# Kernel tuning notes

Measured on AMD Instinct MI355X. Metric: run time of the kernel, lower is better.

## Reference

```python
import jax, jax.numpy as jnp
import numpy as np
from jax import lax

N, E, F, H, B = 16384, 262144, 32, 128, 16
DI, DS, DC, DTR = 256, 16, 4, 8   # Mamba: d_inner=expand*H, d_state, d_conv, dt_rank=ceil(H/16)
NS, NC = 512, 8                   # num_stations, num line colors
EPS = 1e-5


def _forward(node_features, edge_index, batch, W_in, b_in, W_g1, b_g1, W_g2, b_g2,
             W_inproj, conv_w, conv_b, W_xproj, W_dt, b_dt, A_log, D_p, W_out,
             gamma, beta, Wc, bc, Wh, bh, Wt, bt, Wp1, bp1, Wp2, bp2, Wd, bd, Ws, bs):
    def gcn(x, W, b):
        # GCNConv with self-loops and symmetric normalization
        loops = jnp.arange(N)
        s = jnp.concatenate([edge_index[0], loops])
        d = jnp.concatenate([edge_index[1], loops])
        deg = jax.ops.segment_sum(jnp.ones(s.shape[0], x.dtype), d, num_segments=N)
        dinv = jnp.where(deg > 0, lax.rsqrt(deg), 0.0)
        xw = x @ W
        msg = xw[s] * (dinv[s] * dinv[d])[:, None]
        return jax.ops.segment_sum(msg, d, num_segments=N) + b

    h = jax.nn.relu(node_features @ W_in + b_in)
    h = jax.nn.relu(gcn(h, W_g1, b_g1))
    h_gnn = jax.nn.relu(gcn(h, W_g2, b_g2))

    # --- Mamba block over the node sequence (batch dim of 1, seq_len = N) ---
    xz = h_gnn @ W_inproj                      # (N, 2*DI)
    x, z = xz[:, :DI], xz[:, DI:]
    xp = jnp.pad(x, ((DC - 1, 0), (0, 0)))     # causal depthwise conv1d
    xc = conv_b + sum(xp[k:k + N] * conv_w[:, k] for k in range(DC))
    x = jax.nn.silu(xc)
    dbl = x @ W_xproj                          # (N, DTR + 2*DS)
    dt = jax.nn.softplus(dbl[:, :DTR] @ W_dt + b_dt)   # (N, DI)
    Bm = dbl[:, DTR:DTR + DS]                  # (N, DS)
    Cm = dbl[:, DTR + DS:]                     # (N, DS)
    A = -jnp.exp(A_log)                        # (DI, DS)
    dA = jnp.exp(dt[:, :, None] * A[None])     # (N, DI, DS)
    dBx = dt[:, :, None] * Bm[:, None, :] * x[:, :, None]

    def step(hst, t):
        dA_t, dBx_t, C_t = t
        hst = dA_t * hst + dBx_t               # (DI, DS)
        return hst, hst @ C_t                  # (DI,)

    _, ys = lax.scan(step, jnp.zeros((DI, DS), x.dtype), (dA, dBx, Cm))
    y = (ys + D_p * x) * jax.nn.silu(z)
    h_mamba = y @ W_out                        # (N, H)

    # residual + LayerNorm
    hh = h_gnn + h_mamba
    mu = hh.mean(-1, keepdims=True)
    var = ((hh - mu) ** 2).mean(-1, keepdims=True)
    h_final = (hh - mu) * lax.rsqrt(var + EPS) * gamma + beta

    # global_mean_pool per graph
    counts = jax.ops.segment_sum(jnp.ones(N, h_final.dtype), batch, num_segments=B)
    ge = jax.ops.segment_sum(h_final, batch, num_segments=B) / jnp.maximum(counts, 1.0)[:, None]

    # critic + all policy heads, concatenated: [1,4,3,NS,NS,NS,NC]
    return jnp.concatenate([ge @ Wc + bc, ge @ Wh + bh, ge @ Wt + bt,
                            ge @ Wp1 + bp1, ge @ Wp2 + bp2, ge @ Wd + bd,
                            ge @ Ws + bs], axis=-1)


def setup_inputs() -> dict:
    key = jax.random.key(0)
    ks = list(jax.random.split(key, 20))
    p = lambda i, shape, s=0.02: jax.random.normal(ks[i], shape, jnp.float32) * s
    return dict(
        node_features=jax.random.normal(ks[0], (N, F), jnp.float32),
        edge_index=jax.random.randint(ks[1], (2, E), 0, N),
        batch=jnp.sort(jax.random.randint(ks[2], (N,), 0, B)),
        W_in=p(3, (F, H)), b_in=jnp.zeros((H,), jnp.float32),
        W_g1=p(4, (H, H)), b_g1=jnp.zeros((H,), jnp.float32),
        W_g2=p(5, (H, H)), b_g2=jnp.zeros((H,), jnp.float32),
        W_inproj=p(6, (H, 2 * DI)),
        conv_w=p(7, (DI, DC)), conv_b=jnp.zeros((DI,), jnp.float32),
        W_xproj=p(8, (DI, DTR + 2 * DS)),
        W_dt=p(9, (DTR, DI)), b_dt=jnp.full((DI,), -4.0, jnp.float32),
        A_log=jnp.log(jnp.broadcast_to(jnp.arange(1.0, DS + 1.0, dtype=jnp.float32), (DI, DS))),
        D_p=jnp.ones((DI,), jnp.float32),
        W_out=p(10, (DI, H)),
        gamma=jnp.ones((H,), jnp.float32), beta=jnp.zeros((H,), jnp.float32),
        Wc=p(11, (H, 1)), bc=jnp.zeros((1,), jnp.float32),
        Wh=p(12, (H, 4)), bh=jnp.zeros((4,), jnp.float32),
        Wt=p(13, (H, 3)), bt=jnp.zeros((3,), jnp.float32),
        Wp1=p(14, (H, NS)), bp1=jnp.zeros((NS,), jnp.float32),
        Wp2=p(15, (H, NS)), bp2=jnp.zeros((NS,), jnp.float32),
        Wd=p(16, (H, NS)), bd=jnp.zeros((NS,), jnp.float32),
        Ws=p(17, (H, NC)), bs=jnp.zeros((NC,), jnp.float32),
    )


def reference(node_features, edge_index, batch, W_in, b_in, W_g1, b_g1, W_g2, b_g2,
              W_inproj, conv_w, conv_b, W_xproj, W_dt, b_dt, A_log, D_p, W_out,
              gamma, beta, Wc, bc, Wh, bh, Wt, bt, Wp1, bp1, Wp2, bp2, Wd, bd, Ws, bs):
    return _forward(node_features, edge_index, batch, W_in, b_in, W_g1, b_g1, W_g2, b_g2,
                    W_inproj, conv_w, conv_b, W_xproj, W_dt, b_dt, A_log, D_p, W_out,
                    gamma, beta, Wc, bc, Wh, bh, Wt, bt, Wp1, bp1, Wp2, bp2, Wd, bd, Ws, bs)
```

## Files before the change

kernel.cpp:

```cpp
#include <hip/hip_runtime.h>
#include <math.h>

#define NN 16384
#define EE 262144
#define FF 32
#define HH 128
#define BB 16
#define DI 256
#define DS 16
#define DC 4
#define DTR 8
#define OUTW 1552
#define NCH 256
#define CHLEN 64
#define NG 8
#define GL 32

__device__ __forceinline__ float siluf(float v) { return v / (1.f + __expf(-v)); }
__device__ __forceinline__ float softplusf(float v) {
    return fmaxf(v, 0.f) + log1pf(expf(-fabsf(v)));
}

__global__ void deg_kernel(const int* __restrict__ dst, int* __restrict__ cnt) {
    int e = blockIdx.x * blockDim.x + threadIdx.x;
    if (e < EE) atomicAdd(&cnt[dst[e]], 1);
}

__global__ __launch_bounds__(1024) void prefix_kernel(const int* __restrict__ cnt,
                                                      int* __restrict__ rowptr,
                                                      int* __restrict__ cursor,
                                                      float* __restrict__ dinv) {
    __shared__ int part[1024];
    int tid = threadIdx.x;
    int4 c4[4];
#pragma unroll
    for (int j = 0; j < 4; j++) c4[j] = ((const int4*)cnt)[tid * 4 + j];
    int v[16] = {c4[0].x, c4[0].y, c4[0].z, c4[0].w, c4[1].x, c4[1].y, c4[1].z, c4[1].w,
                 c4[2].x, c4[2].y, c4[2].z, c4[2].w, c4[3].x, c4[3].y, c4[3].z, c4[3].w};
    int s = 0;
#pragma unroll
    for (int j = 0; j < 16; j++) s += v[j];
    part[tid] = s;
    __syncthreads();
    for (int off = 1; off < 1024; off <<= 1) {
        int t = (tid >= off) ? part[tid - off] : 0;
        __syncthreads();
        part[tid] += t;
        __syncthreads();
    }
    int running = part[tid] - s;
    int rp[16];
    float dv[16];
#pragma unroll
    for (int j = 0; j < 16; j++) {
        rp[j] = running;
        running += v[j];
        dv[j] = rsqrtf((float)(v[j] + 1));
    }
#pragma unroll
    for (int j = 0; j < 4; j++) {
        int4 r4; r4.x = rp[j*4]; r4.y = rp[j*4+1]; r4.z = rp[j*4+2]; r4.w = rp[j*4+3];
        ((int4*)rowptr)[tid * 4 + j] = r4;
        ((int4*)cursor)[tid * 4 + j] = r4;
        float4 d4; d4.x = dv[j*4]; d4.y = dv[j*4+1]; d4.z = dv[j*4+2]; d4.w = dv[j*4+3];
        ((float4*)dinv)[tid * 4 + j] = d4;
    }
    if (tid == 1023) rowptr[NN] = part[1023];
}

__global__ void scatter_kernel(const int* __restrict__ src, const int* __restrict__ dst,
                               int* __restrict__ cursor, int* __restrict__ col) {
    int e = blockIdx.x * blockDim.x + threadIdx.x;
    if (e < EE) {
        int d = dst[e];
        int pos = atomicAdd(&cursor[d], 1);
        col[pos] = src[e];
    }
}

__global__ __launch_bounds__(256) void gemm_k(const float* __restrict__ A,
                                              const float* __restrict__ B,
                                              const float* __restrict__ bias,
                                              float* __restrict__ C,
                                              int M, int Nn, int K, int act) {
    __shared__ float As[16][68];
    __shared__ float Bs[16][68];
    int tid = threadIdx.x;
    int m0 = blockIdx.y * 64;
    int n0 = blockIdx.x * 64;
    int ty = tid >> 4, tx = tid & 15;
    float acc[4][4] = {{0.f}};
    for (int k0 = 0; k0 < K; k0 += 16) {
#pragma unroll
        for (int l = 0; l < 4; l++) {
            int idx = tid + l * 256;
            int i = idx >> 4, j = idx & 15;
            As[j][i] = A[(size_t)(m0 + i) * K + k0 + j];
        }
#pragma unroll
        for (int l = 0; l < 4; l++) {
            int idx = tid + l * 256;
            int i = idx >> 6, j = idx & 63;
            int n = n0 + j;
            Bs[i][j] = (n < Nn) ? B[(size_t)(k0 + i) * Nn + n] : 0.f;
        }
        __syncthreads();
#pragma unroll
        for (int kk = 0; kk < 16; kk++) {
            float4 a4 = *(const float4*)&As[kk][ty * 4];
            float4 b4 = *(const float4*)&Bs[kk][tx * 4];
            float av[4] = {a4.x, a4.y, a4.z, a4.w};
            float bv[4] = {b4.x, b4.y, b4.z, b4.w};
#pragma unroll
            for (int r = 0; r < 4; r++)
#pragma unroll
                for (int c = 0; c < 4; c++) acc[r][c] = fmaf(av[r], bv[c], acc[r][c]);
        }
        __syncthreads();
    }
    int nb = n0 + tx * 4;
    if (nb < Nn) {
        float4 bi4 = {0.f, 0.f, 0.f, 0.f};
        if (bias) bi4 = *(const float4*)&bias[nb];
#pragma unroll
        for (int r = 0; r < 4; r++) {
            int m = m0 + ty * 4 + r;
            float4 v;
            v.x = acc[r][0] + bi4.x; v.y = acc[r][1] + bi4.y;
            v.z = acc[r][2] + bi4.z; v.w = acc[r][3] + bi4.w;
            if (act == 1) {
                v.x = fmaxf(v.x, 0.f); v.y = fmaxf(v.y, 0.f);
                v.z = fmaxf(v.z, 0.f); v.w = fmaxf(v.w, 0.f);
            }
            *(float4*)&C[(size_t)m * Nn + nb] = v;
        }
    }
}

__global__ __launch_bounds__(256) void gemm_at(const float* __restrict__ AT,
                                               const float* __restrict__ B,
                                               float* __restrict__ C,
                                               int M, int Nn, int K) {
    __shared__ float As[16][68];
    __shared__ float Bs[16][68];
    int tid = threadIdx.x;
    int m0 = blockIdx.y * 64;
    int n0 = blockIdx.x * 64;
    int ty = tid >> 4, tx = tid & 15;
    float acc[4][4] = {{0.f}};
    for (int k0 = 0; k0 < K; k0 += 16) {
#pragma unroll
        for (int l = 0; l < 4; l++) {
            int idx = tid + l * 256;
            int kk = idx >> 6, i = idx & 63;
            As[kk][i] = AT[(size_t)(k0 + kk) * M + m0 + i];
        }
#pragma unroll
        for (int l = 0; l < 4; l++) {
            int idx = tid + l * 256;
            int i = idx >> 6, j = idx & 63;
            int n = n0 + j;
            Bs[i][j] = (n < Nn) ? B[(size_t)(k0 + i) * Nn + n] : 0.f;
        }
        __syncthreads();
#pragma unroll
        for (int kk = 0; kk < 16; kk++) {
            float4 a4 = *(const float4*)&As[kk][ty * 4];
            float4 b4 = *(const float4*)&Bs[kk][tx * 4];
            float av[4] = {a4.x, a4.y, a4.z, a4.w};
            float bv[4] = {b4.x, b4.y, b4.z, b4.w};
#pragma unroll
            for (int r = 0; r < 4; r++)
#pragma unroll
                for (int c = 0; c < 4; c++) acc[r][c] = fmaf(av[r], bv[c], acc[r][c]);
        }
        __syncthreads();
    }
    int nb = n0 + tx * 4;
    if (nb < Nn) {
#pragma unroll
        for (int r = 0; r < 4; r++) {
            int m = m0 + ty * 4 + r;
            float4 v;
            v.x = acc[r][0]; v.y = acc[r][1]; v.z = acc[r][2]; v.w = acc[r][3];
            *(float4*)&C[(size_t)m * Nn + nb] = v;
        }
    }
}

__global__ void gcn_gather(const float* __restrict__ xw, const int* __restrict__ rowptr,
                           const int* __restrict__ col, const float* __restrict__ dinv,
                           const float* __restrict__ b, float* __restrict__ out) {
    int n = blockIdx.x;
    int f = threadIdx.x;
    float dn = dinv[n];
    float acc = xw[(size_t)n * HH + f] * dn * dn;
    int beg = rowptr[n], end = rowptr[n + 1];
    int e = beg;
    for (; e + 4 <= end; e += 4) {
        int s0 = col[e], s1 = col[e + 1], s2 = col[e + 2], s3 = col[e + 3];
        float w0 = dinv[s0] * dn, w1 = dinv[s1] * dn, w2 = dinv[s2] * dn, w3 = dinv[s3] * dn;
        float v0 = xw[(size_t)s0 * HH + f];
        float v1 = xw[(size_t)s1 * HH + f];
        float v2 = xw[(size_t)s2 * HH + f];
        float v3 = xw[(size_t)s3 * HH + f];
        acc = fmaf(v0, w0, acc);
        acc = fmaf(v1, w1, acc);
        acc = fmaf(v2, w2, acc);
        acc = fmaf(v3, w3, acc);
    }
    for (; e < end; e++) {
        int s0 = col[e];
        acc = fmaf(xw[(size_t)s0 * HH + f], dinv[s0] * dn, acc);
    }
    acc += b[f];
    out[(size_t)n * HH + f] = fmaxf(acc, 0.f);
}

__global__ __launch_bounds__(256) void conv_silu_t(const float* __restrict__ xz,
                                                   const float* __restrict__ cw,
                                                   const float* __restrict__ cb,
                                                   float* __restrict__ xst,
                                                   float* __restrict__ szt) {
    __shared__ float tile[67][65];
    int tid = threadIdx.x;
    int t0 = blockIdx.x * 64;
    int c0 = blockIdx.y * 64;
#pragma unroll
    for (int l = 0; l < 17; l++) {
        int idx = tid + l * 256;
        if (idx < 67 * 64) {
            int r = idx >> 6, c = idx & 63;
            int gt = t0 - 3 + r;
            tile[r][c] = (gt >= 0) ? xz[(size_t)gt * 512 + c0 + c] : 0.f;
        }
    }
    __syncthreads();
    int tl = tid & 63;
    int d0 = tid >> 6;
    if (c0 < 256) {
#pragma unroll
        for (int l = 0; l < 16; l++) {
            int dl = d0 + l * 4;
            int dg = c0 + dl;
            float acc = cb[dg];
#pragma unroll
            for (int k = 0; k < DC; k++)
                acc = fmaf(tile[tl + k][dl], cw[dg * DC + k], acc);
            xst[dg * NN + t0 + tl] = siluf(acc);
        }
    } else {
#pragma unroll
        for (int l = 0; l < 16; l++) {
            int dl = d0 + l * 4;
            int dg = c0 - 256 + dl;
            szt[dg * NN + t0 + tl] = siluf(tile[tl + 3][dl]);
        }
    }
}

__global__ __launch_bounds__(256) void transpose_dbl(const float* __restrict__ dbl,
                                                     float* __restrict__ dblt) {
    __shared__ float tile[64][41];
    int tid = threadIdx.x;
    int t0 = blockIdx.x * 64;
#pragma unroll
    for (int l = 0; l < 10; l++) {
        int idx = tid + l * 256;
        int r = idx / 40, c = idx - r * 40;
        tile[r][c] = dbl[(size_t)(t0 + r) * 40 + c];
    }
    __syncthreads();
#pragma unroll
    for (int l = 0; l < 10; l++) {
        int idx = tid + l * 256;
        int c = idx >> 6, t = idx & 63;
        dblt[c * NN + t0 + t] = tile[t][c];
    }
}

__global__ __launch_bounds__(256) void dt_t_kernel(const float* __restrict__ dblt,
                                                   const float* __restrict__ W_dt,
                                                   const float* __restrict__ b_dt,
                                                   float* __restrict__ dtt) {
    int t = blockIdx.x * 256 + threadIdx.x;
    int d = blockIdx.y;
    float acc = b_dt[d];
#pragma unroll
    for (int j = 0; j < DTR; j++)
        acc = fmaf(dblt[j * NN + t], W_dt[j * DI + d], acc);
    dtt[d * NN + t] = softplusf(acc);
}

__global__ __launch_bounds__(256, 8) void scan_phase1(const float* __restrict__ dtt,
                                                      const float* __restrict__ xst,
                                                      const float* __restrict__ dblt,
                                                      const float* __restrict__ A_log,
                                                      float* __restrict__ chkP,
                                                      float* __restrict__ chkH) {
    __shared__ float Td[32][68];
    __shared__ float Tx[32][68];
    __shared__ float Bs[16][68];
    int tid = threadIdx.x;
    int wave = tid >> 6, lane = tid & 63;
    int sg = lane & 7, dl = lane >> 3;
    int dblk = blockIdx.x, chunk = blockIdx.y;
    int t0 = chunk * CHLEN;
    int dloc = wave * 8 + dl;
    int d = dblk * 32 + dloc;
    int s0 = 2 * sg;
#pragma unroll
    for (int p = 0; p < 2; p++) {
        int linear = tid + p * 256;
        int row = linear >> 4, c4 = (linear & 15) * 4;
        *(float4*)&Td[row][c4] = *(const float4*)&dtt[(size_t)(dblk * 32 + row) * NN + t0 + c4];
        *(float4*)&Tx[row][c4] = *(const float4*)&xst[(size_t)(dblk * 32 + row) * NN + t0 + c4];
    }
    {
        int s = tid >> 4, c4 = (tid & 15) * 4;
        *(float4*)&Bs[s][c4] = *(const float4*)&dblt[(size_t)(8 + s) * NN + t0 + c4];
    }
    float A0 = -expf(A_log[d * DS + s0]);
    float A1 = -expf(A_log[d * DS + s0 + 1]);
    __syncthreads();
    float h0 = 0.f, h1 = 0.f, P0 = 1.f, P1 = 1.f;
    for (int i = 0; i < CHLEN; i += 4) {
        float4 d4 = *(const float4*)&Td[dloc][i];
        float4 x4 = *(const float4*)&Tx[dloc][i];
        float4 b04 = *(const float4*)&Bs[s0][i];
        float4 b14 = *(const float4*)&Bs[s0 + 1][i];
#define P1S(U) { float dtv = d4.U; float a0 = __expf(dtv * A0); float a1 = __expf(dtv * A1); \
        float dx = dtv * x4.U; h0 = fmaf(a0, h0, dx * b04.U); h1 = fmaf(a1, h1, dx * b14.U); \
        P0 *= a0; P1 *= a1; }
        P1S(x) P1S(y) P1S(z) P1S(w)
#undef P1S
    }
    int idx = chunk * 4096 + d * DS + s0;
    float2 vP; vP.x = P0; vP.y = P1;
    float2 vH; vH.x = h0; vH.y = h1;
    *(float2*)(chkP + idx) = vP;
    *(float2*)(chkH + idx) = vH;
}

__global__ void scan_phase2a(const float* __restrict__ chkP, const float* __restrict__ chkH,
                             float* __restrict__ gp, float* __restrict__ gh) {
    int g = blockIdx.x * blockDim.x + threadIdx.x;
    int idx = g & 4095;
    int grp = g >> 12;
    int c0 = grp * GL;
    float P = 1.f, H = 0.f;
    for (int j = 0; j < GL; j += 4) {
        float p[4], q[4];
#pragma unroll
        for (int jj = 0; jj < 4; jj++) {
            p[jj] = chkP[(c0 + j + jj) * 4096 + idx];
            q[jj] = chkH[(c0 + j + jj) * 4096 + idx];
        }
#pragma unroll
        for (int jj = 0; jj < 4; jj++) {
            H = fmaf(p[jj], H, q[jj]);
            P *= p[jj];
        }
    }
    gp[grp * 4096 + idx] = P;
    gh[grp * 4096 + idx] = H;
}

__global__ void scan_phase2b(const float* __restrict__ gp, const float* __restrict__ gh,
                             float* __restrict__ gini) {
    int idx = blockIdx.x * blockDim.x + threadIdx.x;
    float h = 0.f;
#pragma unroll
    for (int g = 0; g < NG; g++) {
        gini[g * 4096 + idx] = h;
        h = fmaf(gp[g * 4096 + idx], h, gh[g * 4096 + idx]);
    }
}

__global__ void scan_phase2c(const float* __restrict__ chkP, const float* __restrict__ chkH,
                             const float* __restrict__ gini, float* __restrict__ init) {
    int g = blockIdx.x * blockDim.x + threadIdx.x;
    int idx = g & 4095;
    int grp = g >> 12;
    int c0 = grp * GL;
    float h = gini[grp * 4096 + idx];
    for (int j = 0; j < GL; j += 4) {
        float p[4], q[4];
#pragma unroll
        for (int jj = 0; jj < 4; jj++) {
            p[jj] = chkP[(c0 + j + jj) * 4096 + idx];
            q[jj] = chkH[(c0 + j + jj) * 4096 + idx];
        }
#pragma unroll
        for (int jj = 0; jj < 4; jj++) {
            init[(c0 + j + jj) * 4096 + idx] = h;
            h = fmaf(p[jj], h, q[jj]);
        }
    }
}

__global__ __launch_bounds__(256, 4) void scan_phase3(const float* __restrict__ dtt,
                                                      const float* __restrict__ xst,
                                                      const float* __restrict__ dblt,
                                                      const float* __restrict__ A_log,
                                                      const float* __restrict__ init,
                                                      const float* __restrict__ D_p,
                                                      const float* __restrict__ szt,
                                                      float* __restrict__ yt) {
    __shared__ float Td[32][68];
    __shared__ float Tx[32][68];
    __shared__ float Tz[32][68];
    __shared__ float Bs[16][68];
    __shared__ float Cs[16][68];
    int tid = threadIdx.x;
    int wave = tid >> 6, lane = tid & 63;
    int sg = lane & 7, dl = lane >> 3;
    int dblk = blockIdx.x, chunk = blockIdx.y;
    int t0 = chunk * CHLEN;
    int dloc = wave * 8 + dl;
    int d = dblk * 32 + dloc;
    int s0 = 2 * sg;
#pragma unroll
    for (int p = 0; p < 2; p++) {
        int linear = tid + p * 256;
        int row = linear >> 4, c4 = (linear & 15) * 4;
        *(float4*)&Td[row][c4] = *(const float4*)&dtt[(size_t)(dblk * 32 + row) * NN + t0 + c4];
        *(float4*)&Tx[row][c4] = *(const float4*)&xst[(size_t)(dblk * 32 + row) * NN + t0 + c4];
        *(float4*)&Tz[row][c4] = *(const float4*)&szt[(size_t)(dblk * 32 + row) * NN + t0 + c4];
    }
    {
        int s = tid >> 4, c4 = (tid & 15) * 4;
        *(float4*)&Bs[s][c4] = *(const float4*)&dblt[(size_t)(8 + s) * NN + t0 + c4];
        *(float4*)&Cs[s][c4] = *(const float4*)&dblt[(size_t)(24 + s) * NN + t0 + c4];
    }
    float A0 = -expf(A_log[d * DS + s0]);
    float A1 = -expf(A_log[d * DS + s0 + 1]);
    float Dd = D_p[d];
    float2 ini = *(const float2*)(init + chunk * 4096 + d * DS + s0);
    float h0 = ini.x, h1 = ini.y;
    __syncthreads();
    for (int i = 0; i < CHLEN; i += 4) {
        float4 d4 = *(const float4*)&Td[dloc][i];
        float4 x4 = *(const float4*)&Tx[dloc][i];
        float4 z4 = *(const float4*)&Tz[dloc][i];
        float4 b04 = *(const float4*)&Bs[s0][i];
        float4 b14 = *(const float4*)&Bs[s0 + 1][i];
        float4 c04 = *(const float4*)&Cs[s0][i];
        float4 c14 = *(const float4*)&Cs[s0 + 1][i];
        float4 yv;
#define P3S(U) { float dtv = d4.U; float a0 = __expf(dtv * A0); float a1 = __expf(dtv * A1); \
        float dx = dtv * x4.U; h0 = fmaf(a0, h0, dx * b04.U); h1 = fmaf(a1, h1, dx * b14.U); \
        float c = fmaf(h1, c14.U, h0 * c04.U); \
        c += __shfl_xor(c, 1); c += __shfl_xor(c, 2); c += __shfl_xor(c, 4); \
        yv.U = (c + Dd * x4.U) * z4.U; }
        P3S(x) P3S(y) P3S(z) P3S(w)
#undef P3S
        if (sg == 0) *(float4*)&Td[dloc][i] = yv;
    }
#pragma unroll
    for (int r = 0; r < 8; r++)
        yt[(size_t)(dblk * 32 + wave * 8 + r) * NN + t0 + lane] = Td[wave * 8 + r][lane];
}

__global__ void add_ln(const float* __restrict__ hg, const float* __restrict__ hm,
                       const float* __restrict__ gamma, const float* __restrict__ beta,
                       float* __restrict__ out) {
    int row = blockIdx.x * 4 + (threadIdx.x >> 6);
    int lane = threadIdx.x & 63;
    size_t base = (size_t)row * HH;
    float v0 = hg[base + lane] + hm[base + lane];
    float v1 = hg[base + 64 + lane] + hm[base + 64 + lane];
    float sum = v0 + v1;
#pragma unroll
    for (int m = 32; m >= 1; m >>= 1) sum += __shfl_xor(sum, m);
    float mu = sum * (1.f / 128.f);
    float d0 = v0 - mu, d1 = v1 - mu;
    float vs = d0 * d0 + d1 * d1;
#pragma unroll
    for (int m = 32; m >= 1; m >>= 1) vs += __shfl_xor(vs, m);
    float inv = rsqrtf(vs * (1.f / 128.f) + 1e-5f);
    out[base + lane] = d0 * inv * gamma[lane] + beta[lane];
    out[base + 64 + lane] = d1 * inv * gamma[64 + lane] + beta[64 + lane];
}

__global__ void pool_kernel(const float* __restrict__ hf, const int* __restrict__ batch,
                            float* __restrict__ ge, int* __restrict__ counts) {
    int f = threadIdx.x;
    int r0 = blockIdx.x * 128;
    int gcur = batch[r0];
    float acc = 0.f;
    int cnt = 0;
    for (int i = 0; i < 128; i += 4) {
        int r = r0 + i;
        int g0 = batch[r], g3 = batch[r + 3];
        float v0 = hf[(size_t)r * HH + f];
        float v1 = hf[(size_t)(r + 1) * HH + f];
        float v2 = hf[(size_t)(r + 2) * HH + f];
        float v3 = hf[(size_t)(r + 3) * HH + f];
        if (g0 == gcur && g3 == gcur) {
            acc += (v0 + v1) + (v2 + v3);
            cnt += 4;
        } else {
            int gs[4] = {g0, batch[r + 1], batch[r + 2], g3};
            float vs[4] = {v0, v1, v2, v3};
#pragma unroll
            for (int k = 0; k < 4; k++) {
                if (gs[k] != gcur) {
                    atomicAdd(&ge[gcur * HH + f], acc);
                    if (f == 0) atomicAdd(&counts[gcur], cnt);
                    acc = 0.f; cnt = 0; gcur = gs[k];
                }
                acc += vs[k];
                cnt++;
            }
        }
    }
    atomicAdd(&ge[gcur * HH + f], acc);
    if (f == 0) atomicAdd(&counts[gcur], cnt);
}

__global__ void ge_norm(float* __restrict__ ge, const int* __restrict__ counts) {
    int idx = blockIdx.x * blockDim.x + threadIdx.x;
    if (idx < BB * HH) {
        int b = idx >> 7;
        ge[idx] /= fmaxf((float)counts[b], 1.f);
    }
}

__global__ void heads_kernel(const float* __restrict__ ge,
                             const float* Wc, const float* bc, const float* Wh, const float* bh,
                             const float* Wt, const float* bt, const float* Wp1, const float* bp1,
                             const float* Wp2, const float* bp2, const float* Wd, const float* bd,
                             const float* Ws, const float* bs, float* __restrict__ out) {
    int col = blockIdx.x * blockDim.x + threadIdx.x;
    int b = blockIdx.y;
    if (col >= OUTW) return;
    const float* W; const float* bi; int lc, w;
    if (col < 1)         { W = Wc;  bi = bc;  lc = col;        w = 1; }
    else if (col < 5)    { W = Wh;  bi = bh;  lc = col - 1;    w = 4; }
    else if (col < 8)    { W = Wt;  bi = bt;  lc = col - 5;    w = 3; }
    else if (col < 520)  { W = Wp1; bi = bp1; lc = col - 8;    w = 512; }
    else if (col < 1032) { W = Wp2; bi = bp2; lc = col - 520;  w = 512; }
    else if (col < 1544) { W = Wd;  bi = bd;  lc = col - 1032; w = 512; }
    else                 { W = Ws;  bi = bs;  lc = col - 1544; w = 8; }
    float acc = bi[lc];
#pragma unroll 8
    for (int f = 0; f < HH; f++) acc = fmaf(ge[b * HH + f], W[f * w + lc], acc);
    out[(size_t)b * OUTW + col] = acc;
}

extern "C" void kernel_launch(void* const* d_in, const int* in_sizes, int n_in,
                              void* d_out, int out_size, void* d_ws, size_t ws_size,
                              hipStream_t stream) {
    const float* nf      = (const float*)d_in[0];
    const int*   ei      = (const int*)d_in[1];
    const int*   batch   = (const int*)d_in[2];
    const float* W_in    = (const float*)d_in[3];
    const float* b_in    = (const float*)d_in[4];
    const float* W_g1    = (const float*)d_in[5];
    const float* b_g1    = (const float*)d_in[6];
    const float* W_g2    = (const float*)d_in[7];
    const float* b_g2    = (const float*)d_in[8];
    const float* W_inproj= (const float*)d_in[9];
    const float* conv_w  = (const float*)d_in[10];
    const float* conv_b  = (const float*)d_in[11];
    const float* W_xproj = (const float*)d_in[12];
    const float* W_dt    = (const float*)d_in[13];
    const float* b_dt    = (const float*)d_in[14];
    const float* A_log   = (const float*)d_in[15];
    const float* D_p     = (const float*)d_in[16];
    const float* W_out   = (const float*)d_in[17];
    const float* gamma   = (const float*)d_in[18];
    const float* beta    = (const float*)d_in[19];
    const float* Wc = (const float*)d_in[20]; const float* bc = (const float*)d_in[21];
    const float* Wh = (const float*)d_in[22]; const float* bh = (const float*)d_in[23];
    const float* Wt = (const float*)d_in[24]; const float* bt = (const float*)d_in[25];
    const float* Wp1= (const float*)d_in[26]; const float* bp1= (const float*)d_in[27];
    const float* Wp2= (const float*)d_in[28]; const float* bp2= (const float*)d_in[29];
    const float* Wd = (const float*)d_in[30]; const float* bd = (const float*)d_in[31];
    const float* Ws = (const float*)d_in[32]; const float* bs = (const float*)d_in[33];

    const int* e_src = ei;
    const int* e_dst = ei + EE;

    float* w = (float*)d_ws;
    size_t o = 0;
    float* F0   = w + o; o += (size_t)NN * HH;
    float* F1   = w + o; o += (size_t)NN * HH;
    float* F2   = w + o; o += (size_t)NN * HH;
    float* XZ   = w + o; o += (size_t)NN * 512;
    float* DTT  = XZ;
    float* YT   = XZ + (size_t)NN * DI;
    float* XST  = w + o; o += (size_t)NN * DI;
    float* SZT  = w + o; o += (size_t)NN * DI;
    float* DBL  = w + o; o += (size_t)NN * 40;
    float* DBLT = w + o; o += (size_t)NN * 40;
    float* GE   = w + o; o += BB * HH;
    float* DINV = w + o; o += NN;
    int* ip = (int*)(w + o);
    int* CNT    = ip; ip += NN;
    int* ROWPTR = ip; ip += NN + 1;
    int* CURSOR = ip; ip += NN;
    int* COL    = ip; ip += EE;
    int* COUNTS = ip; ip += BB;

    float* CHP  = F0;
    float* CHH  = F0 + (size_t)NCH * 4096;
    float* INI  = F1;
    float* GP   = DBL;
    float* GH   = DBL + NG * 4096;
    float* GINI = DBL + 2 * NG * 4096;

    hipMemsetAsync(CNT, 0, NN * sizeof(int), stream);
    hipMemsetAsync(GE, 0, BB * HH * sizeof(float), stream);
    hipMemsetAsync(COUNTS, 0, BB * sizeof(int), stream);

    deg_kernel<<<EE / 256, 256, 0, stream>>>(e_dst, CNT);
    prefix_kernel<<<1, 1024, 0, stream>>>(CNT, ROWPTR, CURSOR, DINV);
    scatter_kernel<<<EE / 256, 256, 0, stream>>>(e_src, e_dst, CURSOR, COL);

    gemm_k<<<dim3(2, NN / 64), 256, 0, stream>>>(nf, W_in, b_in, F0, NN, HH, FF, 1);
    gemm_k<<<dim3(2, NN / 64), 256, 0, stream>>>(F0, W_g1, nullptr, F1, NN, HH, HH, 0);
    gcn_gather<<<NN, HH, 0, stream>>>(F1, ROWPTR, COL, DINV, b_g1, F0);
    gemm_k<<<dim3(2, NN / 64), 256, 0, stream>>>(F0, W_g2, nullptr, F1, NN, HH, HH, 0);
    gcn_gather<<<NN, HH, 0, stream>>>(F1, ROWPTR, COL, DINV, b_g2, F2);

    gemm_k<<<dim3(8, NN / 64), 256, 0, stream>>>(F2, W_inproj, nullptr, XZ, NN, 512, HH, 0);
    conv_silu_t<<<dim3(NN / 64, 8), 256, 0, stream>>>(XZ, conv_w, conv_b, XST, SZT);
    gemm_at<<<dim3(1, NN / 64), 256, 0, stream>>>(XST, W_xproj, DBL, NN, 40, DI);
    transpose_dbl<<<NN / 64, 256, 0, stream>>>(DBL, DBLT);
    dt_t_kernel<<<dim3(NN / 256, DI), 256, 0, stream>>>(DBLT, W_dt, b_dt, DTT);

    scan_phase1<<<dim3(8, NCH), 256, 0, stream>>>(DTT, XST, DBLT, A_log, CHP, CHH);
    scan_phase2a<<<(4096 * NG) / 256, 256, 0, stream>>>(CHP, CHH, GP, GH);
    scan_phase2b<<<16, 256, 0, stream>>>(GP, GH, GINI);
    scan_phase2c<<<(4096 * NG) / 256, 256, 0, stream>>>(CHP, CHH, GINI, INI);
    scan_phase3<<<dim3(8, NCH), 256, 0, stream>>>(DTT, XST, DBLT, A_log, INI, D_p, SZT, YT);

    gemm_at<<<dim3(2, NN / 64), 256, 0, stream>>>(YT, W_out, F1, NN, HH, DI);
    add_ln<<<NN / 4, 256, 0, stream>>>(F2, F1, gamma, beta, F0);

    pool_kernel<<<NN / 128, HH, 0, stream>>>(F0, batch, GE, COUNTS);
    ge_norm<<<(BB * HH + 255) / 256, 256, 0, stream>>>(GE, COUNTS);

    heads_kernel<<<dim3((OUTW + 127) / 128, BB), 128, 0, stream>>>(
        GE, Wc, bc, Wh, bh, Wt, bt, Wp1, bp1, Wp2, bp2, Wd, bd, Ws, bs, (float*)d_out);
}
```

Baseline: 450.1 us.

## Fuse dt projection into scan kernels and add 128x128 GEMM for in_proj

```diff
diff --git a/kernel.cpp b/kernel.cpp
--- a/kernel.cpp
+++ b/kernel.cpp
@@ -18,7 +18,7 @@
 
 __device__ __forceinline__ float siluf(float v) { return v / (1.f + __expf(-v)); }
 __device__ __forceinline__ float softplusf(float v) {
-    return fmaxf(v, 0.f) + log1pf(expf(-fabsf(v)));
+    return fmaxf(v, 0.f) + __logf(1.f + __expf(-fabsf(v)));
 }
 
 __global__ void deg_kernel(const int* __restrict__ dst, int* __restrict__ cnt) {
@@ -134,6 +134,63 @@
             }
             *(float4*)&C[(size_t)m * Nn + nb] = v;
         }
+    }
+}
+
+__global__ __launch_bounds__(256, 2) void gemm_big(const float* __restrict__ A,
+                                                   const float* __restrict__ B,
+                                                   float* __restrict__ C,
+                                                   int M, int Nn, int K) {
+    __shared__ float As[16][132];
+    __shared__ float Bs[16][132];
+    int tid = threadIdx.x;
+    int m0 = blockIdx.y * 128;
+    int n0 = blockIdx.x * 128;
+    int ty = tid >> 4, tx = tid & 15;
+    float acc[8][8] = {{0.f}};
+    for (int k0 = 0; k0 < K; k0 += 16) {
+        {
+            int m = tid >> 1;
+            int kc = (tid & 1) * 8;
+            const float* ap = &A[(size_t)(m0 + m) * K + k0 + kc];
+            float4 a0 = *(const float4*)ap;
+            float4 a1 = *(const float4*)(ap + 4);
+            As[kc + 0][m] = a0.x; As[kc + 1][m] = a0.y;
+            As[kc + 2][m] = a0.z; As[kc + 3][m] = a0.w;
+            As[kc + 4][m] = a1.x; As[kc + 5][m] = a1.y;
+            As[kc + 6][m] = a1.z; As[kc + 7][m] = a1.w;
+        }
+        {
+            int krow = tid >> 4;
+            int c8 = (tid & 15) * 8;
+            const float* bp = &B[(size_t)(k0 + krow) * Nn + n0 + c8];
+            *(float4*)&Bs[krow][c8] = *(const float4*)bp;
+            *(float4*)&Bs[krow][c8 + 4] = *(const float4*)(bp + 4);
+        }
+        __syncthreads();
+#pragma unroll
+        for (int kk = 0; kk < 16; kk++) {
+            float4 a0 = *(const float4*)&As[kk][ty * 4];
+            float4 a1 = *(const float4*)&As[kk][64 + ty * 4];
+            float4 b0 = *(const float4*)&Bs[kk][tx * 4];
+            float4 b1 = *(const float4*)&Bs[kk][64 + tx * 4];
+            float av[8] = {a0.x, a0.y, a0.z, a0.w, a1.x, a1.y, a1.z, a1.w};
+            float bv[8] = {b0.x, b0.y, b0.z, b0.w, b1.x, b1.y, b1.z, b1.w};
+#pragma unroll
+            for (int r = 0; r < 8; r++)
+#pragma unroll
+                for (int c = 0; c < 8; c++) acc[r][c] = fmaf(av[r], bv[c], acc[r][c]);
+        }
+        __syncthreads();
+    }
+#pragma unroll
+    for (int r = 0; r < 8; r++) {
+        int m = m0 + ((r < 4) ? (ty * 4 + r) : (64 + ty * 4 + r - 4));
+        float4 v0, v1;
+        v0.x = acc[r][0]; v0.y = acc[r][1]; v0.z = acc[r][2]; v0.w = acc[r][3];
+        v1.x = acc[r][4]; v1.y = acc[r][5]; v1.z = acc[r][6]; v1.w = acc[r][7];
+        *(float4*)&C[(size_t)m * Nn + n0 + tx * 4] = v0;
+        *(float4*)&C[(size_t)m * Nn + n0 + 64 + tx * 4] = v1;
     }
 }
 
@@ -279,28 +336,17 @@
     }
 }
 
-__global__ __launch_bounds__(256) void dt_t_kernel(const float* __restrict__ dblt,
-                                                   const float* __restrict__ W_dt,
-                                                   const float* __restrict__ b_dt,
-                                                   float* __restrict__ dtt) {
-    int t = blockIdx.x * 256 + threadIdx.x;
-    int d = blockIdx.y;
-    float acc = b_dt[d];
-#pragma unroll
-    for (int j = 0; j < DTR; j++)
-        acc = fmaf(dblt[j * NN + t], W_dt[j * DI + d], acc);
-    dtt[d * NN + t] = softplusf(acc);
-}
-
-__global__ __launch_bounds__(256, 8) void scan_phase1(const float* __restrict__ dtt,
-                                                      const float* __restrict__ xst,
+__global__ __launch_bounds__(256, 6) void scan_phase1(const float* __restrict__ xst,
                                                       const float* __restrict__ dblt,
                                                       const float* __restrict__ A_log,
+                                                      const float* __restrict__ W_dt,
+                                                      const float* __restrict__ b_dt,
                                                       float* __restrict__ chkP,
                                                       float* __restrict__ chkH) {
     __shared__ float Td[32][68];
     __shared__ float Tx[32][68];
     __shared__ float Bs[16][68];
+    __shared__ float D8[8][68];
     int tid = threadIdx.x;
     int wave = tid >> 6, lane = tid & 63;
     int sg = lane & 7, dl = lane >> 3;
@@ -313,8 +359,11 @@
     for (int p = 0; p < 2; p++) {
         int linear = tid + p * 256;
         int row = linear >> 4, c4 = (linear & 15) * 4;
-        *(float4*)&Td[row][c4] = *(const float4*)&dtt[(size_t)(dblk * 32 + row) * NN + t0 + c4];
         *(float4*)&Tx[row][c4] = *(const float4*)&xst[(size_t)(dblk * 32 + row) * NN + t0 + c4];
+    }
+    if (tid < 128) {
+        int r = tid >> 4, c4 = (tid & 15) * 4;
+        *(float4*)&D8[r][c4] = *(const float4*)&dblt[(size_t)r * NN + t0 + c4];
     }
     {
         int s = tid >> 4, c4 = (tid & 15) * 4;
@@ -322,6 +371,24 @@
     }
     float A0 = -expf(A_log[d * DS + s0]);
     float A1 = -expf(A_log[d * DS + s0 + 1]);
+    __syncthreads();
+    {
+        int row = tid >> 3;
+        int tb = (tid & 7) * 8;
+        int dd = dblk * 32 + row;
+        float bd = b_dt[dd];
+        float wv[8];
+#pragma unroll
+        for (int j = 0; j < 8; j++) wv[j] = W_dt[j * DI + dd];
+#pragma unroll
+        for (int j = 0; j < 8; j++) {
+            int t = tb + j;
+            float acc = bd;
+#pragma unroll
+            for (int k = 0; k < 8; k++) acc = fmaf(D8[k][t], wv[k], acc);
+            Td[row][t] = softplusf(acc);
+        }
+    }
     __syncthreads();
     float h0 = 0.f, h1 = 0.f, P0 = 1.f, P1 = 1.f;
     for (int i = 0; i < CHLEN; i += 4) {
@@ -399,19 +466,20 @@
     }
 }
 
-__global__ __launch_bounds__(256, 4) void scan_phase3(const float* __restrict__ dtt,
-                                                      const float* __restrict__ xst,
+__global__ __launch_bounds__(256, 5) void scan_phase3(const float* __restrict__ xst,
                                                       const float* __restrict__ dblt,
                                                       const float* __restrict__ A_log,
+                                                      const float* __restrict__ W_dt,
+                                                      const float* __restrict__ b_dt,
                                                       const float* __restrict__ init,
                                                       const float* __restrict__ D_p,
                                                       const float* __restrict__ szt,
                                                       float* __restrict__ yt) {
     __shared__ float Td[32][68];
     __shared__ float Tx[32][68];
-    __shared__ float Tz[32][68];
     __shared__ float Bs[16][68];
     __shared__ float Cs[16][68];
+    __shared__ float D8[8][68];
     int tid = threadIdx.x;
     int wave = tid >> 6, lane = tid & 63;
     int sg = lane & 7, dl = lane >> 3;
@@ -424,9 +492,11 @@
     for (int p = 0; p < 2; p++) {
         int linear = tid + p * 256;
         int row = linear >> 4, c4 = (linear & 15) * 4;
-        *(float4*)&Td[row][c4] = *(const float4*)&dtt[(size_t)(dblk * 32 + row) * NN + t0 + c4];
         *(float4*)&Tx[row][c4] = *(const float4*)&xst[(size_t)(dblk * 32 + row) * NN + t0 + c4];
-        *(float4*)&Tz[row][c4] = *(const float4*)&szt[(size_t)(dblk * 32 + row) * NN + t0 + c4];
+    }
+    if (tid < 128) {
+        int r = tid >> 4, c4 = (tid & 15) * 4;
+        *(float4*)&D8[r][c4] = *(const float4*)&dblt[(size_t)r * NN + t0 + c4];
     }
     {
         int s = tid >> 4, c4 = (tid & 15) * 4;
@@ -439,10 +509,27 @@
     float2 ini = *(const float2*)(init + chunk * 4096 + d * DS + s0);
     float h0 = ini.x, h1 = ini.y;
     __syncthreads();
+    {
+        int row = tid >> 3;
+        int tb = (tid & 7) * 8;
+        int dd = dblk * 32 + row;
+        float bd = b_dt[dd];
+        float wv[8];
+#pragma unroll
+        for (int j = 0; j < 8; j++) wv[j] = W_dt[j * DI + dd];
+#pragma unroll
+        for (int j = 0; j < 8; j++) {
+            int t = tb + j;
+            float acc = bd;
+#pragma unroll
+            for (int k = 0; k < 8; k++) acc = fmaf(D8[k][t], wv[k], acc);
+            Td[row][t] = softplusf(acc);
+        }
+    }
+    __syncthreads();
     for (int i = 0; i < CHLEN; i += 4) {
         float4 d4 = *(const float4*)&Td[dloc][i];
         float4 x4 = *(const float4*)&Tx[dloc][i];
-        float4 z4 = *(const float4*)&Tz[dloc][i];
         float4 b04 = *(const float4*)&Bs[s0][i];
         float4 b14 = *(const float4*)&Bs[s0 + 1][i];
         float4 c04 = *(const float4*)&Cs[s0][i];
@@ -452,14 +539,17 @@
         float dx = dtv * x4.U; h0 = fmaf(a0, h0, dx * b04.U); h1 = fmaf(a1, h1, dx * b14.U); \
         float c = fmaf(h1, c14.U, h0 * c04.U); \
         c += __shfl_xor(c, 1); c += __shfl_xor(c, 2); c += __shfl_xor(c, 4); \
-        yv.U = (c + Dd * x4.U) * z4.U; }
+        yv.U = c + Dd * x4.U; }
         P3S(x) P3S(y) P3S(z) P3S(w)
 #undef P3S
         if (sg == 0) *(float4*)&Td[dloc][i] = yv;
     }
 #pragma unroll
-    for (int r = 0; r < 8; r++)
-        yt[(size_t)(dblk * 32 + wave * 8 + r) * NN + t0 + lane] = Td[wave * 8 + r][lane];
+    for (int r = 0; r < 8; r++) {
+        int row = wave * 8 + r;
+        float sz = szt[(size_t)(dblk * 32 + row) * NN + t0 + lane];
+        yt[(size_t)(dblk * 32 + row) * NN + t0 + lane] = Td[row][lane] * sz;
+    }
 }
 
 __global__ void add_ln(const float* __restrict__ hg, const float* __restrict__ hm,
@@ -589,8 +679,7 @@
     float* F1   = w + o; o += (size_t)NN * HH;
     float* F2   = w + o; o += (size_t)NN * HH;
     float* XZ   = w + o; o += (size_t)NN * 512;
-    float* DTT  = XZ;
-    float* YT   = XZ + (size_t)NN * DI;
+    float* YT   = XZ;
     float* XST  = w + o; o += (size_t)NN * DI;
     float* SZT  = w + o; o += (size_t)NN * DI;
     float* DBL  = w + o; o += (size_t)NN * 40;
@@ -625,17 +714,16 @@
     gemm_k<<<dim3(2, NN / 64), 256, 0, stream>>>(F0, W_g2, nullptr, F1, NN, HH, HH, 0);
     gcn_gather<<<NN, HH, 0, stream>>>(F1, ROWPTR, COL, DINV, b_g2, F2);
 
-    gemm_k<<<dim3(8, NN / 64), 256, 0, stream>>>(F2, W_inproj, nullptr, XZ, NN, 512, HH, 0);
+    gemm_big<<<dim3(4, NN / 128), 256, 0, stream>>>(F2, W_inproj, XZ, NN, 512, HH);
     conv_silu_t<<<dim3(NN / 64, 8), 256, 0, stream>>>(XZ, conv_w, conv_b, XST, SZT);
     gemm_at<<<dim3(1, NN / 64), 256, 0, stream>>>(XST, W_xproj, DBL, NN, 40, DI);
     transpose_dbl<<<NN / 64, 256, 0, stream>>>(DBL, DBLT);
-    dt_t_kernel<<<dim3(NN / 256, DI), 256, 0, stream>>>(DBLT, W_dt, b_dt, DTT);
-
-    scan_phase1<<<dim3(8, NCH), 256, 0, stream>>>(DTT, XST, DBLT, A_log, CHP, CHH);
+
+    scan_phase1<<<dim3(8, NCH), 256, 0, stream>>>(XST, DBLT, A_log, W_dt, b_dt, CHP, CHH);
     scan_phase2a<<<(4096 * NG) / 256, 256, 0, stream>>>(CHP, CHH, GP, GH);
     scan_phase2b<<<16, 256, 0, stream>>>(GP, GH, GINI);
     scan_phase2c<<<(4096 * NG) / 256, 256, 0, stream>>>(CHP, CHH, GINI, INI);
-    scan_phase3<<<dim3(8, NCH), 256, 0, stream>>>(DTT, XST, DBLT, A_log, INI, D_p, SZT, YT);
+    scan_phase3<<<dim3(8, NCH), 256, 0, stream>>>(XST, DBLT, A_log, W_dt, b_dt, INI, D_p, SZT, YT);
 
     gemm_at<<<dim3(2, NN / 64), 256, 0, stream>>>(YT, W_out, F1, NN, HH, DI);
     add_ln<<<NN / 4, 256, 0, stream>>>(F2, F1, gamma, beta, F0);
```

Result: no change. 449.0 us (-0.3%).
